# Optimization experiments

Hardware: AMD Instinct MI355X
Metric: run time of the kernel (lower is better)

Reference implementation:

```python
import jax, jax.numpy as jnp
import numpy as np

N = 50000      # nodes
E = 800000     # edges (avg degree 16)
D = 128        # node_dim
H = 128        # hidden_dim
ED = 16        # edge_dim (unused by GCNConv, kept for signature fidelity)
G = 64         # graphs in batch
EPS = 1e-5     # BatchNorm eps


def setup_inputs() -> dict:
    key = jax.random.key(0)
    ks = jax.random.split(key, 16)
    s = 0.05
    inp = {
        "x": jax.random.normal(ks[0], (N, D), jnp.float32),
        "edge_index": jax.random.randint(ks[1], (2, E), 0, N, dtype=jnp.int64),
        "edge_attr": jax.random.normal(ks[2], (E, ED), jnp.float32),
        "batch": jnp.sort(jax.random.randint(ks[3], (N,), 0, G, dtype=jnp.int64)),
        # GCNConv weights/biases
        "W1": jax.random.normal(ks[4], (D, H), jnp.float32) * s,
        "b1": jnp.zeros((H,), jnp.float32),
        "W2": jax.random.normal(ks[5], (H, H), jnp.float32) * s,
        "b2": jnp.zeros((H,), jnp.float32),
        "W3": jax.random.normal(ks[6], (H, H), jnp.float32) * s,
        "b3": jnp.zeros((H,), jnp.float32),
        # BatchNorm affine params (training-mode batch stats)
        "g1": jnp.ones((H,), jnp.float32), "be1": jnp.zeros((H,), jnp.float32),
        "g2": jnp.ones((H,), jnp.float32), "be2": jnp.zeros((H,), jnp.float32),
        "g3": jnp.ones((H,), jnp.float32), "be3": jnp.zeros((H,), jnp.float32),
    }
    return inp


def reference(x, edge_index, edge_attr, batch,
              W1, b1, W2, b2, W3, b3,
              g1, be1, g2, be2, g3, be3):
    n = x.shape[0]
    src, dst = edge_index[0], edge_index[1]

    # GCN symmetric normalization with added self-loops:
    # deg[i] = 1 + in_degree(i); norm(e) = deg[src]^-1/2 * deg[dst]^-1/2
    deg = jax.ops.segment_sum(jnp.ones((src.shape[0],), x.dtype), dst,
                              num_segments=n) + 1.0
    dinv = jax.lax.rsqrt(deg)
    edge_norm = (dinv[src] * dinv[dst])[:, None]   # [E,1]
    self_norm = (dinv * dinv)[:, None]             # [N,1] self-loop weight

    def gcn(h, W, b):
        h = h @ W                                  # [N,H]
        agg = jax.ops.segment_sum(h[src] * edge_norm, dst, num_segments=n)
        return agg + h * self_norm + b

    def bn_sigmoid(h, g, b):
        m = h.mean(0)
        v = jnp.mean(jnp.square(h - m), 0)         # biased variance (torch BN)
        return jax.nn.sigmoid((h - m) * jax.lax.rsqrt(v + EPS) * g + b)

    h = bn_sigmoid(gcn(x, W1, b1), g1, be1)
    h = bn_sigmoid(gcn(h, W2, b2), g2, be2)
    h = bn_sigmoid(gcn(h, W3, b3), g3, be3)

    # global_mean_pool over graph ids
    cnt = jax.ops.segment_sum(jnp.ones((n,), h.dtype), batch, num_segments=G)
    pooled = jax.ops.segment_sum(h, batch, num_segments=G)
    return pooled / jnp.maximum(cnt, 1.0)[:, None]
```

## Files before the change

kernel.cpp:

```cpp
#include <hip/hip_runtime.h>
#include <math.h>

#define NDIM 128

typedef __attribute__((ext_vector_type(8))) short short8;
typedef __attribute__((ext_vector_type(4))) float f32x4;

__device__ __forceinline__ float sigmoidf_(float x){ return 1.0f/(1.0f + __expf(-x)); }

__device__ __forceinline__ unsigned short f2bf(float f){
  unsigned u = __float_as_uint(f);
  unsigned r = (u + 0x7fffu + ((u >> 16) & 1u)) >> 16;
  return (unsigned short)r;
}
__device__ __forceinline__ float bflo(unsigned u){ return __uint_as_float(u<<16); }
__device__ __forceinline__ float bfhi(unsigned u){ return __uint_as_float(u & 0xffff0000u); }

__global__ void init_k(int* __restrict__ counts, float* __restrict__ sums,
                       float* __restrict__ out, int N, int outsz){
  int i = blockIdx.x*256 + threadIdx.x;
  if(i < N) counts[i] = 0;
  if(i < 2*3*128) sums[i] = 0.f;
  if(i < outsz) out[i] = 0.f;
}

__global__ void pass1_k(const int* __restrict__ dst, int* __restrict__ counts,
                        int* __restrict__ rank, int E){
  int e = blockIdx.x*blockDim.x + threadIdx.x;
  if(e < E) rank[e] = atomicAdd(&counts[dst[e]], 1);
}

__global__ void scan1_k(const int* __restrict__ counts, int* __restrict__ scanned,
                        int* __restrict__ chunksums, int N){
  __shared__ int lds[256];
  int t = threadIdx.x; int idx = blockIdx.x*256 + t;
  int x = (idx < N) ? counts[idx] : 0;
  lds[t] = x; __syncthreads();
  for(int o=1;o<256;o<<=1){
    int v = (t>=o) ? lds[t-o] : 0;
    __syncthreads();
    lds[t] += v;
    __syncthreads();
  }
  if(idx < N) scanned[idx] = lds[t];
  if(t == 255) chunksums[blockIdx.x] = lds[255];
}

__global__ void scan3_k(const int* __restrict__ scanned, const int* __restrict__ counts,
                        const int* __restrict__ chunksums, int* __restrict__ row_start,
                        float* __restrict__ dinv, int N, int nchunks){
  __shared__ int lds[256];
  int t = threadIdx.x, b = blockIdx.x;
  int x = (t < nchunks) ? chunksums[t] : 0;
  lds[t] = x; __syncthreads();
  for(int o=1;o<256;o<<=1){
    int v = (t>=o) ? lds[t-o] : 0;
    __syncthreads();
    lds[t] += v;
    __syncthreads();
  }
  int base = (b == 0) ? 0 : lds[b-1];
  int i = b*256 + t;
  if(i < N){
    row_start[i] = scanned[i] - counts[i] + base;
    dinv[i] = rsqrtf(1.0f + (float)counts[i]);
  }
}

__global__ void pass2_k(const int* __restrict__ src, const int* __restrict__ dst,
                        const int* __restrict__ rank, const int* __restrict__ row_start,
                        unsigned short* __restrict__ csr, int E){
  int e = blockIdx.x*blockDim.x + threadIdx.x;
  if(e >= E) return;
  csr[row_start[dst[e]] + rank[e]] = (unsigned short)src[e];
}

__global__ void wprep_k(const float* __restrict__ W0, const float* __restrict__ W1,
                        const float* __restrict__ W2, unsigned short* __restrict__ Wsw,
                        const int* __restrict__ batch, int* __restrict__ bound,
                        int N, int G){
  int t = blockIdx.x*256 + threadIdx.x;
  if(t < 3*16384){
    int l = t >> 14; int i = t & 16383;
    const float* W = (l==0) ? W0 : ((l==1) ? W1 : W2);
    int k = i >> 7, n = i & 127;
    Wsw[l*16384 + (((k>>3)*128 + n)<<3) + (k&7)] = f2bf(W[k*128+n]);
  } else {
    int g = t - 3*16384;
    if(g <= G){
      int lo = 0, hi = N;
      while(lo < hi){ int mid = (lo+hi)>>1; if(batch[mid] < g) lo = mid+1; else hi = mid; }
      bound[g] = lo;
    }
  }
}

__global__ __launch_bounds__(256) void gemm_mfma_k(const void* __restrict__ Avoid,
                                                   const unsigned short* __restrict__ Wsw,
                                                   unsigned short* __restrict__ Bh,
                                                   const float* __restrict__ dinv,
                                                   const float* __restrict__ sums,
                                                   const float* __restrict__ sumsq,
                                                   const float* __restrict__ gam,
                                                   const float* __restrict__ bet,
                                                   int N){
  __shared__ unsigned short Al[16384];
  __shared__ unsigned short Wl[16384];
  __shared__ float scl[NDIM], shl[NDIM], dvl[NDIM];
  int t = threadIdx.x;
  int row0 = blockIdx.x * 128;
  bool bn = (sums != nullptr);

  if(bn && t < NDIM){
    float invN = 1.0f/(float)N;
    float m = sums[t]*invN;
    float var = fmaxf(sumsq[t]*invN - m*m, 0.f);
    float s = gam[t]*rsqrtf(var + 1e-5f);
    scl[t] = s; shl[t] = bet[t] - m*s;
  }
  if(t < NDIM){
    int r = row0 + t;
    dvl[t] = (r < N) ? dinv[r] : 0.f;
  }
  #pragma unroll
  for(int i=0;i<8;i++){
    int u = t + i*256;
    *(uint4*)&Wl[u<<3] = *(const uint4*)&Wsw[u<<3];
  }
  __syncthreads();

  int o = t & 15, rbase = t >> 4;
  if(bn){
    const unsigned* Ab = (const unsigned*)Avoid;
    #pragma unroll
    for(int it=0; it<8; it++){
      int r = rbase + it*16;
      int grow = row0 + r;
      uint4 pk = {0,0,0,0};
      if(grow < N){
        uint4 pb = *(const uint4*)&Ab[(size_t)grow*64 + o*4];
        float a0=bflo(pb.x), a1=bfhi(pb.x), a2=bflo(pb.y), a3=bfhi(pb.y);
        float a4=bflo(pb.z), a5=bfhi(pb.z), a6=bflo(pb.w), a7=bfhi(pb.w);
        int f = o*8;
        a0 = sigmoidf_(a0*scl[f+0] + shl[f+0]);
        a1 = sigmoidf_(a1*scl[f+1] + shl[f+1]);
        a2 = sigmoidf_(a2*scl[f+2] + shl[f+2]);
        a3 = sigmoidf_(a3*scl[f+3] + shl[f+3]);
        a4 = sigmoidf_(a4*scl[f+4] + shl[f+4]);
        a5 = sigmoidf_(a5*scl[f+5] + shl[f+5]);
        a6 = sigmoidf_(a6*scl[f+6] + shl[f+6]);
        a7 = sigmoidf_(a7*scl[f+7] + shl[f+7]);
        pk.x = (unsigned)f2bf(a0) | ((unsigned)f2bf(a1)<<16);
        pk.y = (unsigned)f2bf(a2) | ((unsigned)f2bf(a3)<<16);
        pk.z = (unsigned)f2bf(a4) | ((unsigned)f2bf(a5)<<16);
        pk.w = (unsigned)f2bf(a6) | ((unsigned)f2bf(a7)<<16);
      }
      *(uint4*)&Al[(o*128 + r)<<3] = pk;
    }
  } else {
    const float* A = (const float*)Avoid;
    #pragma unroll
    for(int it=0; it<8; it++){
      int r = rbase + it*16;
      int grow = row0 + r;
      uint4 pk = {0,0,0,0};
      if(grow < N){
        float4 v0 = *(const float4*)&A[(size_t)grow*NDIM + o*8];
        float4 v1 = *(const float4*)&A[(size_t)grow*NDIM + o*8 + 4];
        pk.x = (unsigned)f2bf(v0.x) | ((unsigned)f2bf(v0.y)<<16);
        pk.y = (unsigned)f2bf(v0.z) | ((unsigned)f2bf(v0.w)<<16);
        pk.z = (unsigned)f2bf(v1.x) | ((unsigned)f2bf(v1.y)<<16);
        pk.w = (unsigned)f2bf(v1.z) | ((unsigned)f2bf(v1.w)<<16);
      }
      *(uint4*)&Al[(o*128 + r)<<3] = pk;
    }
  }
  __syncthreads();

  int wv = t >> 6, lane = t & 63, quad = lane >> 4, l16 = lane & 15;
  int rw = (wv & 1) * 64, cw = (wv >> 1) * 64;
  f32x4 acc[4][4];
  #pragma unroll
  for(int rt=0;rt<4;rt++)
    #pragma unroll
    for(int ct=0;ct<4;ct++) acc[rt][ct] = (f32x4){0.f,0.f,0.f,0.f};

  #pragma unroll
  for(int ks=0; ks<4; ks++){
    short8 a[4], b[4];
    #pragma unroll
    for(int rt=0;rt<4;rt++)
      a[rt] = *(short8*)&Al[(((ks*4+quad)*128) + rw + rt*16 + l16) << 3];
    #pragma unroll
    for(int ct=0;ct<4;ct++)
      b[ct] = *(short8*)&Wl[(((ks*4+quad)*128) + cw + ct*16 + l16) << 3];
    #pragma unroll
    for(int rt=0;rt<4;rt++)
      #pragma unroll
      for(int ct=0;ct<4;ct++)
        acc[rt][ct] = __builtin_amdgcn_mfma_f32_16x16x32_bf16(a[rt], b[ct], acc[rt][ct], 0, 0, 0);
  }

  #pragma unroll
  for(int rt=0;rt<4;rt++){
    int lr = rw + rt*16 + quad*4;
    int gr = row0 + lr;
    #pragma unroll
    for(int reg=0;reg<4;reg++){
      float dv = dvl[lr + reg];
      if(gr + reg < N){
        #pragma unroll
        for(int ct=0;ct<4;ct++){
          int col = cw + ct*16 + l16;
          Bh[(size_t)(gr+reg)*NDIM + col] = f2bf(acc[rt][ct][reg]*dv);
        }
      }
    }
  }
}

__global__ __launch_bounds__(256) void agg_k(const unsigned int* __restrict__ hb,
                      const float* __restrict__ dinv,
                      const int* __restrict__ row_start, const int* __restrict__ counts,
                      const unsigned short* __restrict__ csr,
                      const float* __restrict__ bias, unsigned int* __restrict__ hCb, int N){
  int t = threadIdx.x;
  int lane = t & 63;
  int i = blockIdx.x*4 + (t >> 6);
  if(i >= N) return;
  int rs = row_start[i], re = rs + counts[i];
  float ax = 0.f, ay = 0.f;
  int j = rs;
  for(; j+7 < re; j += 8){
    int s0=csr[j],   s1=csr[j+1], s2=csr[j+2], s3=csr[j+3];
    int s4=csr[j+4], s5=csr[j+5], s6=csr[j+6], s7=csr[j+7];
    unsigned u0 = hb[(size_t)s0*64 + lane];
    unsigned u1 = hb[(size_t)s1*64 + lane];
    unsigned u2 = hb[(size_t)s2*64 + lane];
    unsigned u3 = hb[(size_t)s3*64 + lane];
    unsigned u4 = hb[(size_t)s4*64 + lane];
    unsigned u5 = hb[(size_t)s5*64 + lane];
    unsigned u6 = hb[(size_t)s6*64 + lane];
    unsigned u7 = hb[(size_t)s7*64 + lane];
    ax += bflo(u0)+bflo(u1)+bflo(u2)+bflo(u3)+bflo(u4)+bflo(u5)+bflo(u6)+bflo(u7);
    ay += bfhi(u0)+bfhi(u1)+bfhi(u2)+bfhi(u3)+bfhi(u4)+bfhi(u5)+bfhi(u6)+bfhi(u7);
  }
  for(; j < re; j++){
    unsigned u0 = hb[(size_t)csr[j]*64 + lane];
    ax += bflo(u0);
    ay += bfhi(u0);
  }
  float di = dinv[i];
  unsigned su = hb[(size_t)i*64 + lane];
  float2 bv = *(const float2*)&bias[lane*2];
  float ox = di*(ax + bflo(su)) + bv.x;
  float oy = di*(ay + bfhi(su)) + bv.y;
  hCb[(size_t)i*64 + lane] = (unsigned)f2bf(ox) | ((unsigned)f2bf(oy)<<16);
}

__global__ void stats_k(const unsigned* __restrict__ hb, float* __restrict__ sums,
                        float* __restrict__ sumsq, int N){
  __shared__ float ls[256], lq[256];
  int t = threadIdx.x;
  int f = t & 127, half = t >> 7;
  int rowsPerBlock = (N + gridDim.x - 1)/gridDim.x;
  int r0 = blockIdx.x * rowsPerBlock;
  int r1 = min(N, r0 + rowsPerBlock);
  float s=0.f, q=0.f;
  for(int r=r0+half; r<r1; r+=2){
    unsigned u = hb[(size_t)r*64 + (f>>1)];
    float v = (f&1) ? bfhi(u) : bflo(u);
    s += v; q += v*v;
  }
  ls[t]=s; lq[t]=q; __syncthreads();
  if(t < 128){
    s = ls[t] + ls[t+128];
    q = lq[t] + lq[t+128];
    atomicAdd(&sums[f], s);
    atomicAdd(&sumsq[f], q);
  }
}

#define PCH 128
__global__ __launch_bounds__(256) void pool_k(const unsigned* __restrict__ hb,
                                              const int* __restrict__ batch,
                                              const float* __restrict__ sums,
                                              const float* __restrict__ sumsq,
                                              const float* __restrict__ gam,
                                              const float* __restrict__ bet,
                                              float* __restrict__ out, int N){
  __shared__ float scl[NDIM], shl[NDIM];
  int t = threadIdx.x;
  if(t < NDIM){
    float invN = 1.0f/(float)N;
    float m = sums[t]*invN;
    float var = fmaxf(sumsq[t]*invN - m*m, 0.f);
    float s = gam[t]*rsqrtf(var + 1e-5f);
    scl[t] = s; shl[t] = bet[t] - m*s;
  }
  __syncthreads();
  int f = t & 127, half = t >> 7;
  int r0 = blockIdx.x*PCH + half;
  int r1 = min(N, blockIdx.x*PCH + PCH);
  float sc = scl[f], sh = shl[f];
  float acc = 0.f; int cur = -1;
  for(int r = r0; r < r1; r += 2){
    int g = batch[r];
    if(g != cur){
      if(cur >= 0) atomicAdd(&out[cur*NDIM + f], acc);
      acc = 0.f; cur = g;
    }
    unsigned u = hb[(size_t)r*64 + (f>>1)];
    float v = (f&1) ? bfhi(u) : bflo(u);
    acc += sigmoidf_(v*sc + sh);
  }
  if(cur >= 0) atomicAdd(&out[cur*NDIM + f], acc);
}

__global__ void div_k(float* __restrict__ out, const int* __restrict__ bound){
  int g = blockIdx.x, f = threadIdx.x;
  float cnt = (float)(bound[g+1] - bound[g]);
  out[g*NDIM + f] /= fmaxf(cnt, 1.0f);
}

extern "C" void kernel_launch(void* const* d_in, const int* in_sizes, int n_in,
                              void* d_out, int out_size, void* d_ws, size_t ws_size,
                              hipStream_t stream){
  const float* x     = (const float*)d_in[0];
  const int*   ei    = (const int*)d_in[1];
  const int*   batch = (const int*)d_in[3];
  const float* W [3] = {(const float*)d_in[4], (const float*)d_in[6], (const float*)d_in[8]};
  const float* bi[3] = {(const float*)d_in[5], (const float*)d_in[7], (const float*)d_in[9]};
  const float* gg[3] = {(const float*)d_in[10], (const float*)d_in[12], (const float*)d_in[14]};
  const float* bb[3] = {(const float*)d_in[11], (const float*)d_in[13], (const float*)d_in[15]};

  int N = in_sizes[0] / NDIM;
  int E = in_sizes[1] / 2;
  int G = out_size / NDIM;
  const int* src = ei;
  const int* dst = ei + E;

  char* p = (char*)d_ws;
  auto alloc = [&](size_t bytes)->void*{
    void* r = (void*)p; p += (bytes + 255) & ~(size_t)255; return r;
  };
  unsigned short* hB  = (unsigned short*)alloc((size_t)N*NDIM*2);
  unsigned*       hCb = (unsigned*)      alloc((size_t)N*64*4);
  unsigned short* Wsw = (unsigned short*)alloc(3*16384*2);
  int*   counts    = (int*)  alloc((size_t)N*4);
  int*   rank      = (int*)  alloc((size_t)E*4);
  int*   scanned   = (int*)  alloc((size_t)N*4);
  int*   chunksums = (int*)  alloc(256*4);
  int*   row_start = (int*)  alloc((size_t)N*4);
  float* dinv      = (float*)alloc((size_t)N*4);
  unsigned short* csr = (unsigned short*)alloc((size_t)E*2);
  float* sums      = (float*)alloc(2*3*128*4);
  float* sumsq     = sums + 3*128;
  int*   bound     = (int*)  alloc(256*4);

  int initmax = (N > out_size) ? N : out_size;
  init_k<<<(initmax+255)/256, 256, 0, stream>>>(counts, sums, (float*)d_out, N, out_size);

  pass1_k<<<(E+255)/256, 256, 0, stream>>>(dst, counts, rank, E);

  int nchunks = (N+255)/256;
  scan1_k<<<nchunks, 256, 0, stream>>>(counts, scanned, chunksums, N);
  scan3_k<<<nchunks, 256, 0, stream>>>(scanned, counts, chunksums, row_start, dinv, N, nchunks);
  pass2_k<<<(E+255)/256, 256, 0, stream>>>(src, dst, rank, row_start, csr, E);
  wprep_k<<<(3*16384+256+255)/256, 256, 0, stream>>>(W[0], W[1], W[2], Wsw, batch, bound, N, G);

  const void* hin = (const void*)x;
  for(int l=0; l<3; l++){
    const float* sm = (l == 0) ? nullptr : (sums  + (l-1)*128);
    const float* sq = (l == 0) ? nullptr : (sumsq + (l-1)*128);
    const float* gm = (l == 0) ? nullptr : gg[l-1];
    const float* be = (l == 0) ? nullptr : bb[l-1];
    gemm_mfma_k<<<(N+127)/128, 256, 0, stream>>>(hin, Wsw + l*16384, hB, dinv,
                                                 sm, sq, gm, be, N);
    agg_k<<<(N+3)/4, 256, 0, stream>>>((const unsigned int*)hB, dinv, row_start, counts,
                                       csr, bi[l], hCb, N);
    stats_k<<<400, 256, 0, stream>>>(hCb, sums + l*128, sumsq + l*128, N);
    hin = (const void*)hCb;
  }

  pool_k<<<(N+PCH-1)/PCH, 256, 0, stream>>>(hCb, batch, sums + 2*128, sumsq + 2*128,
                                            gg[2], bb[2], (float*)d_out, N);
  div_k<<<G, 128, 0, stream>>>((float*)d_out, bound);
}
```

Measured before the change: 458.7 us.

## Fuse BatchNorm stats into aggregation kernel and merge weight prep into init

```diff
diff --git a/kernel.cpp b/kernel.cpp
--- a/kernel.cpp
+++ b/kernel.cpp
@@ -16,12 +16,30 @@
 __device__ __forceinline__ float bflo(unsigned u){ return __uint_as_float(u<<16); }
 __device__ __forceinline__ float bfhi(unsigned u){ return __uint_as_float(u & 0xffff0000u); }
 
-__global__ void init_k(int* __restrict__ counts, float* __restrict__ sums,
-                       float* __restrict__ out, int N, int outsz){
+
+__global__ void init_k(int* __restrict__ counts, float* __restrict__ stats,
+                       float* __restrict__ out,
+                       const float* __restrict__ W0, const float* __restrict__ W1,
+                       const float* __restrict__ W2, unsigned short* __restrict__ Wsw,
+                       const int* __restrict__ batch, int* __restrict__ bound,
+                       int N, int outsz, int G){
   int i = blockIdx.x*256 + threadIdx.x;
   if(i < N) counts[i] = 0;
-  if(i < 2*3*128) sums[i] = 0.f;
+  if(i < 3*8192) stats[i] = 0.f;
   if(i < outsz) out[i] = 0.f;
+  int d = i - N;
+  if(d >= 0 && d < 3*16384){
+    int l = d >> 14; int ii = d & 16383;
+    const float* W = (l==0) ? W0 : ((l==1) ? W1 : W2);
+    int k = ii >> 7, n = ii & 127;
+    Wsw[l*16384 + (((k>>3)*128 + n)<<3) + (k&7)] = f2bf(W[k*128+n]);
+  }
+  int g = i - N - 3*16384;
+  if(g >= 0 && g <= G){
+    int lo = 0, hi = N;
+    while(lo < hi){ int mid = (lo+hi)>>1; if(batch[mid] < g) lo = mid+1; else hi = mid; }
+    bound[g] = lo;
+  }
 }
 
 __global__ void pass1_k(const int* __restrict__ dst, int* __restrict__ counts,
@@ -75,32 +93,11 @@
   csr[row_start[dst[e]] + rank[e]] = (unsigned short)src[e];
 }
 
-__global__ void wprep_k(const float* __restrict__ W0, const float* __restrict__ W1,
-                        const float* __restrict__ W2, unsigned short* __restrict__ Wsw,
-                        const int* __restrict__ batch, int* __restrict__ bound,
-                        int N, int G){
-  int t = blockIdx.x*256 + threadIdx.x;
-  if(t < 3*16384){
-    int l = t >> 14; int i = t & 16383;
-    const float* W = (l==0) ? W0 : ((l==1) ? W1 : W2);
-    int k = i >> 7, n = i & 127;
-    Wsw[l*16384 + (((k>>3)*128 + n)<<3) + (k&7)] = f2bf(W[k*128+n]);
-  } else {
-    int g = t - 3*16384;
-    if(g <= G){
-      int lo = 0, hi = N;
-      while(lo < hi){ int mid = (lo+hi)>>1; if(batch[mid] < g) lo = mid+1; else hi = mid; }
-      bound[g] = lo;
-    }
-  }
-}
-
 __global__ __launch_bounds__(256) void gemm_mfma_k(const void* __restrict__ Avoid,
                                                    const unsigned short* __restrict__ Wsw,
                                                    unsigned short* __restrict__ Bh,
                                                    const float* __restrict__ dinv,
-                                                   const float* __restrict__ sums,
-                                                   const float* __restrict__ sumsq,
+                                                   const float* __restrict__ stats,
                                                    const float* __restrict__ gam,
                                                    const float* __restrict__ bet,
                                                    int N){
@@ -109,12 +106,12 @@
   __shared__ float scl[NDIM], shl[NDIM], dvl[NDIM];
   int t = threadIdx.x;
   int row0 = blockIdx.x * 128;
-  bool bn = (sums != nullptr);
+  bool bn = (stats != nullptr);
 
   if(bn && t < NDIM){
     float invN = 1.0f/(float)N;
-    float m = sums[t]*invN;
-    float var = fmaxf(sumsq[t]*invN - m*m, 0.f);
+    float m = stats[t*32]*invN;
+    float var = fmaxf(stats[t*32+16]*invN - m*m, 0.f);
     float s = gam[t]*rsqrtf(var + 1e-5f);
     scl[t] = s; shl[t] = bet[t] - m*s;
   }
@@ -219,73 +216,71 @@
   }
 }
 
+#define AGG_GRID 1024
 __global__ __launch_bounds__(256) void agg_k(const unsigned int* __restrict__ hb,
                       const float* __restrict__ dinv,
                       const int* __restrict__ row_start, const int* __restrict__ counts,
                       const unsigned short* __restrict__ csr,
-                      const float* __restrict__ bias, unsigned int* __restrict__ hCb, int N){
+                      const float* __restrict__ bias, unsigned int* __restrict__ hCb,
+                      float* __restrict__ stats, int N){
+  __shared__ float se[256], so[256], qe[256], qo[256];
   int t = threadIdx.x;
-  int lane = t & 63;
-  int i = blockIdx.x*4 + (t >> 6);
-  if(i >= N) return;
-  int rs = row_start[i], re = rs + counts[i];
-  float ax = 0.f, ay = 0.f;
-  int j = rs;
-  for(; j+7 < re; j += 8){
-    int s0=csr[j],   s1=csr[j+1], s2=csr[j+2], s3=csr[j+3];
-    int s4=csr[j+4], s5=csr[j+5], s6=csr[j+6], s7=csr[j+7];
-    unsigned u0 = hb[(size_t)s0*64 + lane];
-    unsigned u1 = hb[(size_t)s1*64 + lane];
-    unsigned u2 = hb[(size_t)s2*64 + lane];
-    unsigned u3 = hb[(size_t)s3*64 + lane];
-    unsigned u4 = hb[(size_t)s4*64 + lane];
-    unsigned u5 = hb[(size_t)s5*64 + lane];
-    unsigned u6 = hb[(size_t)s6*64 + lane];
-    unsigned u7 = hb[(size_t)s7*64 + lane];
-    ax += bflo(u0)+bflo(u1)+bflo(u2)+bflo(u3)+bflo(u4)+bflo(u5)+bflo(u6)+bflo(u7);
-    ay += bfhi(u0)+bfhi(u1)+bfhi(u2)+bfhi(u3)+bfhi(u4)+bfhi(u5)+bfhi(u6)+bfhi(u7);
-  }
-  for(; j < re; j++){
-    unsigned u0 = hb[(size_t)csr[j]*64 + lane];
-    ax += bflo(u0);
-    ay += bfhi(u0);
-  }
-  float di = dinv[i];
-  unsigned su = hb[(size_t)i*64 + lane];
+  int lane = t & 63, w = t >> 6;
   float2 bv = *(const float2*)&bias[lane*2];
-  float ox = di*(ax + bflo(su)) + bv.x;
-  float oy = di*(ay + bfhi(su)) + bv.y;
-  hCb[(size_t)i*64 + lane] = (unsigned)f2bf(ox) | ((unsigned)f2bf(oy)<<16);
-}
-
-__global__ void stats_k(const unsigned* __restrict__ hb, float* __restrict__ sums,
-                        float* __restrict__ sumsq, int N){
-  __shared__ float ls[256], lq[256];
-  int t = threadIdx.x;
-  int f = t & 127, half = t >> 7;
-  int rowsPerBlock = (N + gridDim.x - 1)/gridDim.x;
-  int r0 = blockIdx.x * rowsPerBlock;
-  int r1 = min(N, r0 + rowsPerBlock);
-  float s=0.f, q=0.f;
-  for(int r=r0+half; r<r1; r+=2){
-    unsigned u = hb[(size_t)r*64 + (f>>1)];
-    float v = (f&1) ? bfhi(u) : bflo(u);
-    s += v; q += v*v;
-  }
-  ls[t]=s; lq[t]=q; __syncthreads();
-  if(t < 128){
-    s = ls[t] + ls[t+128];
-    q = lq[t] + lq[t+128];
-    atomicAdd(&sums[f], s);
-    atomicAdd(&sumsq[f], q);
+  float sx = 0.f, sy = 0.f, qx = 0.f, qy = 0.f;
+
+  for(int i = blockIdx.x*4 + w; i < N; i += gridDim.x*4){
+    int rs = row_start[i], re = rs + counts[i];
+    float ax = 0.f, ay = 0.f;
+    int j = rs;
+    for(; j+7 < re; j += 8){
+      int s0=csr[j],   s1=csr[j+1], s2=csr[j+2], s3=csr[j+3];
+      int s4=csr[j+4], s5=csr[j+5], s6=csr[j+6], s7=csr[j+7];
+      unsigned u0 = hb[(size_t)s0*64 + lane];
+      unsigned u1 = hb[(size_t)s1*64 + lane];
+      unsigned u2 = hb[(size_t)s2*64 + lane];
+      unsigned u3 = hb[(size_t)s3*64 + lane];
+      unsigned u4 = hb[(size_t)s4*64 + lane];
+      unsigned u5 = hb[(size_t)s5*64 + lane];
+      unsigned u6 = hb[(size_t)s6*64 + lane];
+      unsigned u7 = hb[(size_t)s7*64 + lane];
+      ax += bflo(u0)+bflo(u1)+bflo(u2)+bflo(u3)+bflo(u4)+bflo(u5)+bflo(u6)+bflo(u7);
+      ay += bfhi(u0)+bfhi(u1)+bfhi(u2)+bfhi(u3)+bfhi(u4)+bfhi(u5)+bfhi(u6)+bfhi(u7);
+    }
+    for(; j < re; j++){
+      unsigned u0 = hb[(size_t)csr[j]*64 + lane];
+      ax += bflo(u0);
+      ay += bfhi(u0);
+    }
+    float di = dinv[i];
+    unsigned su = hb[(size_t)i*64 + lane];
+    float ox = di*(ax + bflo(su)) + bv.x;
+    float oy = di*(ay + bfhi(su)) + bv.y;
+    hCb[(size_t)i*64 + lane] = (unsigned)f2bf(ox) | ((unsigned)f2bf(oy)<<16);
+    sx += ox; qx += ox*ox;
+    sy += oy; qy += oy*oy;
+  }
+
+  se[t] = sx; so[t] = sy; qe[t] = qx; qo[t] = qy;
+  __syncthreads();
+  if(t < 64){
+    float s = se[t]+se[t+64]+se[t+128]+se[t+192];
+    float q = qe[t]+qe[t+64]+qe[t+128]+qe[t+192];
+    atomicAdd(&stats[(2*t)*32],      s);
+    atomicAdd(&stats[(2*t)*32 + 16], q);
+  } else if(t < 128){
+    int l = t - 64;
+    float s = so[l]+so[l+64]+so[l+128]+so[l+192];
+    float q = qo[l]+qo[l+64]+qo[l+128]+qo[l+192];
+    atomicAdd(&stats[(2*l+1)*32],      s);
+    atomicAdd(&stats[(2*l+1)*32 + 16], q);
   }
 }
 
 #define PCH 128
 __global__ __launch_bounds__(256) void pool_k(const unsigned* __restrict__ hb,
                                               const int* __restrict__ batch,
-                                              const float* __restrict__ sums,
-                                              const float* __restrict__ sumsq,
+                                              const float* __restrict__ stats,
                                               const float* __restrict__ gam,
                                               const float* __restrict__ bet,
                                               float* __restrict__ out, int N){
@@ -293,8 +288,8 @@
   int t = threadIdx.x;
   if(t < NDIM){
     float invN = 1.0f/(float)N;
-    float m = sums[t]*invN;
-    float var = fmaxf(sumsq[t]*invN - m*m, 0.f);
+    float m = stats[t*32]*invN;
+    float var = fmaxf(stats[t*32+16]*invN - m*m, 0.f);
     float s = gam[t]*rsqrtf(var + 1e-5f);
     scl[t] = s; shl[t] = bet[t] - m*s;
   }
@@ -354,12 +349,13 @@
   int*   row_start = (int*)  alloc((size_t)N*4);
   float* dinv      = (float*)alloc((size_t)N*4);
   unsigned short* csr = (unsigned short*)alloc((size_t)E*2);
-  float* sums      = (float*)alloc(2*3*128*4);
-  float* sumsq     = sums + 3*128;
+  float* stats     = (float*)alloc((size_t)3*8192*4);
   int*   bound     = (int*)  alloc(256*4);
 
-  int initmax = (N > out_size) ? N : out_size;
-  init_k<<<(initmax+255)/256, 256, 0, stream>>>(counts, sums, (float*)d_out, N, out_size);
+  int initmax = N + 3*16384 + G + 1;
+  init_k<<<(initmax+255)/256, 256, 0, stream>>>(counts, stats, (float*)d_out,
+                                                W[0], W[1], W[2], Wsw, batch, bound,
+                                                N, out_size, G);
 
   pass1_k<<<(E+255)/256, 256, 0, stream>>>(dst, counts, rank, E);
 
@@ -367,23 +363,20 @@
   scan1_k<<<nchunks, 256, 0, stream>>>(counts, scanned, chunksums, N);
   scan3_k<<<nchunks, 256, 0, stream>>>(scanned, counts, chunksums, row_start, dinv, N, nchunks);
   pass2_k<<<(E+255)/256, 256, 0, stream>>>(src, dst, rank, row_start, csr, E);
-  wprep_k<<<(3*16384+256+255)/256, 256, 0, stream>>>(W[0], W[1], W[2], Wsw, batch, bound, N, G);
 
   const void* hin = (const void*)x;
   for(int l=0; l<3; l++){
-    const float* sm = (l == 0) ? nullptr : (sums  + (l-1)*128);
-    const float* sq = (l == 0) ? nullptr : (sumsq + (l-1)*128);
+    const float* st = (l == 0) ? nullptr : (stats + (l-1)*8192);
     const float* gm = (l == 0) ? nullptr : gg[l-1];
     const float* be = (l == 0) ? nullptr : bb[l-1];
     gemm_mfma_k<<<(N+127)/128, 256, 0, stream>>>(hin, Wsw + l*16384, hB, dinv,
-                                                 sm, sq, gm, be, N);
-    agg_k<<<(N+3)/4, 256, 0, stream>>>((const unsigned int*)hB, dinv, row_start, counts,
-                                       csr, bi[l], hCb, N);
-    stats_k<<<400, 256, 0, stream>>>(hCb, sums + l*128, sumsq + l*128, N);
+                                                 st, gm, be, N);
+    agg_k<<<AGG_GRID, 256, 0, stream>>>((const unsigned int*)hB, dinv, row_start, counts,
+                                        csr, bi[l], hCb, stats + l*8192, N);
     hin = (const void*)hCb;
   }
 
-  pool_k<<<(N+PCH-1)/PCH, 256, 0, stream>>>(hCb, batch, sums + 2*128, sumsq + 2*128,
+  pool_k<<<(N+PCH-1)/PCH, 256, 0, stream>>>(hCb, batch, stats + 2*8192,
                                             gg[2], bb[2], (float*)d_out, N);
   div_k<<<G, 128, 0, stream>>>((float*)d_out, bound);
 }
```

Result: slower. 479.5 us (+4.5%).
